# Optimization experiments

Hardware: AMD Instinct MI355X
Metric: run time of the kernel (lower is better)

The kernel has to match this reference:

```python
import jax, jax.numpy as jnp
import numpy as np

# Architecture constants (match init_kwargs)
NUM_INPUTS = 3      # 2 spatial + 1 time
NUM_SPATIAL = NUM_INPUTS - 1
NUM_LAYERS = 4      # hidden Linear(H,H) blocks
HIDDEN = 256
N_POINTS = 131072
M_DIFF = 1.0        # scalar conductivity M


def setup_inputs() -> dict:
    key = jax.random.key(0)
    ks = jax.random.split(key, 5)
    X = jax.random.uniform(ks[0], (N_POINTS, NUM_INPUTS), dtype=jnp.float32)
    # Xavier-normal weights, zero biases (matches init_method='xavier')
    W_in = jax.random.normal(ks[1], (NUM_INPUTS, HIDDEN), dtype=jnp.float32) * np.sqrt(2.0 / (NUM_INPUTS + HIDDEN))
    b_in = jnp.zeros((HIDDEN,), dtype=jnp.float32)
    W_h = jax.random.normal(ks[2], (NUM_LAYERS, HIDDEN, HIDDEN), dtype=jnp.float32) * np.sqrt(2.0 / (2 * HIDDEN))
    b_h = jnp.zeros((NUM_LAYERS, HIDDEN), dtype=jnp.float32)
    W_out = jax.random.normal(ks[3], (HIDDEN, 1), dtype=jnp.float32) * np.sqrt(2.0 / (HIDDEN + 1))
    b_out = jnp.zeros((1,), dtype=jnp.float32)
    return {"X_collocation": X, "W_in": W_in, "b_in": b_in,
            "W_h": W_h, "b_h": b_h, "W_out": W_out, "b_out": b_out}


def reference(X_collocation, W_in, b_in, W_h, b_h, W_out, b_out):
    """Faithful translation of MonodomainSolverPINNs.pde with use_ode=False,
    scalar M, no source term: residual = dv/dt - M * Laplacian_spatial(v).
    Returns (pde_loss, ode_loss)."""

    def mlp_scalar(x):  # x: [NUM_INPUTS] -> scalar v
        h = jnp.tanh(x @ W_in + b_in)
        for i in range(NUM_LAYERS):  # static small loop over layers
            h = jnp.tanh(h @ W_h[i] + b_h[i])
        return (h @ W_out + b_out)[0]

    grad_fn = jax.grad(mlp_scalar)

    def derivs(x):
        # forward-over-reverse: one reverse pass for grad, one JVP per spatial dim
        g = grad_fn(x)                       # [NUM_INPUTS]
        diag = []
        for i in range(NUM_SPATIAL):
            e = jnp.zeros((NUM_INPUTS,), dtype=x.dtype).at[i].set(1.0)
            _, hv = jax.jvp(grad_fn, (x,), (e,))
            diag.append(hv[i])               # d^2v/dx_i^2
        return g[-1], jnp.stack(diag).sum()  # dv/dt, spatial laplacian

    dv_dt, laplacian = jax.vmap(derivs)(X_collocation)  # each [N]
    diffusion = M_DIFF * laplacian
    residual = dv_dt - diffusion                        # reaction term = 0
    pde_loss = jnp.mean(residual ** 2)
    ode_loss = jnp.float32(0.0)
    return (pde_loss, ode_loss)
```

## Files before the change

kernel.cpp:

```cpp
#include <hip/hip_runtime.h>
#include <hip/hip_bf16.h>

typedef __attribute__((ext_vector_type(8))) short  short8;
typedef __attribute__((ext_vector_type(4))) float  f32x4;

#define HIDDEN   256
#define NLAYERS  4
#define NPTS     131072
#define PPW      16
#define NWG      (NPTS / PPW)
#define NSTATE   5
#define PLANE    40960

#define WS_PARTIALS   0
#define WS_WHI        65536

__device__ __forceinline__ unsigned short f2bf(float f) {
    return __builtin_bit_cast(unsigned short, __float2bfloat16(f));
}
__device__ __forceinline__ float bf2f(unsigned short h) {
    return __uint_as_float(((unsigned)h) << 16);
}
__device__ __forceinline__ unsigned pack2(float a, float b) {
    __hip_bfloat162 h2 = __float22bfloat162_rn(make_float2(a, b));
    unsigned u;
    __builtin_memcpy(&u, &h2, sizeof(u));
    return u;
}
__device__ __forceinline__ float fast_tanh(float z) {
    float e = __expf(2.f * z);
    return 1.f - __fdividef(2.f, e + 1.f);
}

__global__ void prep_w(const float* __restrict__ Wh, unsigned short* __restrict__ whi)
{
    int b    = blockIdx.x;
    int lay  = b >> 7;
    int jt   = (b >> 3) & 15;
    int kt   = b & 7;
    int lane = threadIdx.x;
    int j    = jt * 16 + (lane & 15);
    int k0   = kt * 32 + (lane >> 4) * 8;
    const float* W = Wh + lay * 65536;
    int base = ((lay * 16 + jt) * 8 + kt) * 512 + lane * 8;
#pragma unroll
    for (int e = 0; e < 8; ++e)
        whi[base + e] = f2bf(W[(k0 + e) * HIDDEN + j]);
}

__global__ __launch_bounds__(512, 4)
void pinn_mfma(const float* __restrict__ X,
               const float* __restrict__ W_in, const float* __restrict__ b_in,
               const float* __restrict__ b_h,  const float* __restrict__ W_out,
               const unsigned short* __restrict__ whi,
               double* __restrict__ partials)
{
    extern __shared__ char lds[];
    char*   P0  = lds;
    char*   P1  = lds + PLANE;
    float*  red = (float*)P1;
    double* sq  = (double*)(P1 + 2048);

    const int tid  = threadIdx.x;
    const int lane = tid & 63;
    const int swid = __builtin_amdgcn_readfirstlane(tid >> 6);
    const int q    = lane >> 4;
    const int p_   = lane & 15;
    const int wg   = blockIdx.x;
    const int pt0  = wg * PPW;

    {
        const int p   = tid & 15;
        const int jq0 = tid >> 4;
        const float* xp = X + (pt0 + p) * 3;
        const float x0 = xp[0], x1 = xp[1], x2 = xp[2];
#pragma unroll
        for (int i = 0; i < 2; ++i) {
            const int jq = jq0 + 32 * i;
            const int j0 = jq * 4;
            const f32x4 w0 = *(const f32x4*)(W_in + j0);
            const f32x4 w1 = *(const f32x4*)(W_in + HIDDEN + j0);
            const f32x4 w2 = *(const f32x4*)(W_in + 2 * HIDDEN + j0);
            const f32x4 bq = *(const f32x4*)(b_in + j0);
            float o[NSTATE][4];
#pragma unroll
            for (int r = 0; r < 4; ++r) {
                float z  = fmaf(x0, w0[r], fmaf(x1, w1[r], fmaf(x2, w2[r], bq[r])));
                float a  = fast_tanh(z);
                float td = 1.f - a * a;
                float m2 = -2.f * a * td;
                o[0][r] = a; o[1][r] = td * w0[r]; o[2][r] = td * w1[r]; o[3][r] = td * w2[r];
                o[4][r] = m2 * fmaf(w0[r], w0[r], w1[r] * w1[r]);
            }
            const int kt = j0 >> 5, kg = (j0 >> 3) & 3, e0 = j0 & 7;
            const int sub = (kg * 16 + p) * 16 + e0 * 2;
#pragma unroll
            for (int s = 0; s < NSTATE; ++s) {
                uint2 w2v = { pack2(o[s][0], o[s][1]), pack2(o[s][2], o[s][3]) };
                *(uint2*)(P0 + (s * 8 + kt) * 1024 + sub) = w2v;
            }
        }
    }
    __syncthreads();

#pragma unroll 1
    for (int l = 0; l < NLAYERS; ++l) {
        char* SP  = (l & 1) ? P1 : P0;
        char* SPn = (l & 1) ? P0 : P1;
        const char* sbase = SP + lane * 16;
        const unsigned short* wbh = whi + (l * 16 + swid * 2) * 4096 + lane * 8;

        f32x4 bias[2];
#pragma unroll
        for (int jj = 0; jj < 2; ++jj)
            bias[jj] = *(const f32x4*)(b_h + l * HIDDEN + (swid * 2 + jj) * 16 + q * 4);

        f32x4 acc[2][NSTATE];
#pragma unroll
        for (int jj = 0; jj < 2; ++jj)
#pragma unroll
            for (int mt = 0; mt < NSTATE; ++mt)
                acc[jj][mt] = (f32x4){0.f, 0.f, 0.f, 0.f};

#pragma unroll 2
        for (int kt = 0; kt < 8; ++kt) {
            short8 wh[2];
#pragma unroll
            for (int jj = 0; jj < 2; ++jj)
                wh[jj] = *(const short8*)(wbh + jj * 4096 + kt * 512);
            short8 sh_[NSTATE];
#pragma unroll
            for (int mt = 0; mt < NSTATE; ++mt)
                sh_[mt] = *(const short8*)(sbase + (mt * 8 + kt) * 1024);

            __builtin_amdgcn_s_setprio(1);
#pragma unroll
            for (int jj = 0; jj < 2; ++jj)
#pragma unroll
                for (int mt = 0; mt < NSTATE; ++mt)
                    acc[jj][mt] = __builtin_amdgcn_mfma_f32_16x16x32_bf16(wh[jj], sh_[mt], acc[jj][mt], 0, 0, 0);
            __builtin_amdgcn_s_setprio(0);
        }


#pragma unroll
        for (int jj = 0; jj < 2; ++jj) {
            const int j0 = (swid * 2 + jj) * 16 + q * 4;
            const int kt = j0 >> 5, kg = (j0 >> 3) & 3, e0 = j0 & 7;
            const int sub = (kg * 16 + p_) * 16 + e0 * 2;
            float o[NSTATE][4];
#pragma unroll
            for (int r = 0; r < 4; ++r) {
                float z0 = acc[jj][0][r] + bias[jj][r];
                float z1 = acc[jj][1][r], z2 = acc[jj][2][r];
                float z3 = acc[jj][3][r], zS = acc[jj][4][r];
                float a  = fast_tanh(z0);
                float td = 1.f - a * a;
                float m2 = -2.f * a * td;
                o[0][r] = a; o[1][r] = td * z1; o[2][r] = td * z2; o[3][r] = td * z3;
                o[4][r] = fmaf(td, zS, m2 * fmaf(z1, z1, z2 * z2));
            }
            const int sLo = (l < NLAYERS - 1) ? 0 : 3;
#pragma unroll
            for (int s = 0; s < NSTATE; ++s) {
                if (s < sLo) continue;
                uint2 w2v = { pack2(o[s][0], o[s][1]), pack2(o[s][2], o[s][3]) };
                *(uint2*)(SPn + (s * 8 + kt) * 1024 + sub) = w2v;
            }
        }
        __syncthreads();
    }

    {
        const int p   = tid & 15;
        const int jq0 = tid >> 4;
        float sum = 0.f;
#pragma unroll
        for (int i = 0; i < 2; ++i) {
            const int jq = jq0 + 32 * i, j0 = jq * 4;
            const int kt = j0 >> 5, kg = (j0 >> 3) & 3, e0 = j0 & 7;
            const int sub = (kg * 16 + p) * 16 + e0 * 2;
            uint2 gv = *(uint2*)(P0 + (3 * 8 + kt) * 1024 + sub);
            uint2 Sv = *(uint2*)(P0 + (4 * 8 + kt) * 1024 + sub);
            f32x4 wo = *(const f32x4*)(W_out + j0);
            sum = fmaf(wo[0], bf2f((unsigned short)(gv.x & 0xFFFF)) - bf2f((unsigned short)(Sv.x & 0xFFFF)), sum);
            sum = fmaf(wo[1], bf2f((unsigned short)(gv.x >> 16))    - bf2f((unsigned short)(Sv.x >> 16)),    sum);
            sum = fmaf(wo[2], bf2f((unsigned short)(gv.y & 0xFFFF)) - bf2f((unsigned short)(Sv.y & 0xFFFF)), sum);
            sum = fmaf(wo[3], bf2f((unsigned short)(gv.y >> 16))    - bf2f((unsigned short)(Sv.y >> 16)),    sum);
        }
        red[jq0 * 16 + p] = sum;
    }
    __syncthreads();
    if (tid < PPW) {
        float s = 0.f;
        for (int g = 0; g < 32; ++g) s += red[g * 16 + tid];
        double d = (double)s;
        sq[tid] = d * d;
    }
    __syncthreads();
    if (tid == 0) {
        double tot = 0.0;
        for (int p = 0; p < PPW; ++p) tot += sq[p];
        partials[wg] = tot;
    }
}

__global__ void pinn_reduce_kernel(const double* __restrict__ partials, float* __restrict__ out)
{
    __shared__ double sh[256];
    double t = 0.0;
    for (int i = 0; i < NWG / 256; ++i) t += partials[threadIdx.x * (NWG / 256) + i];
    sh[threadIdx.x] = t;
    __syncthreads();
    for (int ofs = 128; ofs > 0; ofs >>= 1) {
        if ((int)threadIdx.x < ofs) sh[threadIdx.x] += sh[threadIdx.x + ofs];
        __syncthreads();
    }
    if (threadIdx.x == 0) {
        out[0] = (float)(sh[0] / (double)NPTS);
        out[1] = 0.f;
    }
}

extern "C" void kernel_launch(void* const* d_in, const int* in_sizes, int n_in,
                              void* d_out, int out_size, void* d_ws, size_t ws_size,
                              hipStream_t stream)
{
    const float* X     = (const float*)d_in[0];
    const float* W_in  = (const float*)d_in[1];
    const float* b_in  = (const float*)d_in[2];
    const float* W_h   = (const float*)d_in[3];
    const float* b_h   = (const float*)d_in[4];
    const float* W_out = (const float*)d_in[5];

    double*         partials = (double*)((char*)d_ws + WS_PARTIALS);
    unsigned short* whi      = (unsigned short*)((char*)d_ws + WS_WHI);
    float*          out      = (float*)d_out;

    const size_t lds_bytes = 2 * PLANE;
    (void)hipFuncSetAttribute((const void*)pinn_mfma,
                              hipFuncAttributeMaxDynamicSharedMemorySize, (int)lds_bytes);

    hipLaunchKernelGGL(prep_w, dim3(512), dim3(64), 0, stream, W_h, whi);
    hipLaunchKernelGGL(pinn_mfma, dim3(NWG), dim3(512), lds_bytes, stream,
                       X, W_in, b_in, b_h, W_out, whi, partials);
    hipLaunchKernelGGL(pinn_reduce_kernel, dim3(1), dim3(256), 0, stream,
                       partials, out);
}
```

Baseline: 368.9 us.

## Fold time-derivative and Laplacian into one tangent state, single-buffer LDS

```diff
diff --git a/kernel.cpp b/kernel.cpp
--- a/kernel.cpp
+++ b/kernel.cpp
@@ -9,8 +9,8 @@
 #define NPTS     131072
 #define PPW      16
 #define NWG      (NPTS / PPW)
-#define NSTATE   5
-#define PLANE    40960
+#define NSTATE   4
+#define PLANE    32768
 
 #define WS_PARTIALS   0
 #define WS_WHI        65536
@@ -48,7 +48,7 @@
         whi[base + e] = f2bf(W[(k0 + e) * HIDDEN + j]);
 }
 
-__global__ __launch_bounds__(512, 4)
+__global__ __launch_bounds__(512, 6)
 void pinn_mfma(const float* __restrict__ X,
                const float* __restrict__ W_in, const float* __restrict__ b_in,
                const float* __restrict__ b_h,  const float* __restrict__ W_out,
@@ -56,10 +56,8 @@
                double* __restrict__ partials)
 {
     extern __shared__ char lds[];
-    char*   P0  = lds;
-    char*   P1  = lds + PLANE;
-    float*  red = (float*)P1;
-    double* sq  = (double*)(P1 + 2048);
+    float*  red = (float*)lds;
+    double* sq  = (double*)(lds + 2048);
 
     const int tid  = threadIdx.x;
     const int lane = tid & 63;
@@ -88,16 +86,19 @@
                 float z  = fmaf(x0, w0[r], fmaf(x1, w1[r], fmaf(x2, w2[r], bq[r])));
                 float a  = fast_tanh(z);
                 float td = 1.f - a * a;
-                float m2 = -2.f * a * td;
-                o[0][r] = a; o[1][r] = td * w0[r]; o[2][r] = td * w1[r]; o[3][r] = td * w2[r];
-                o[4][r] = m2 * fmaf(w0[r], w0[r], w1[r] * w1[r]);
+                float t2 = 2.f * a * td;
+                float sw = fmaf(w0[r], w0[r], w1[r] * w1[r]);
+                o[0][r] = a;
+                o[1][r] = td * w0[r];
+                o[2][r] = td * w1[r];
+                o[3][r] = fmaf(td, w2[r], t2 * sw);
             }
             const int kt = j0 >> 5, kg = (j0 >> 3) & 3, e0 = j0 & 7;
             const int sub = (kg * 16 + p) * 16 + e0 * 2;
 #pragma unroll
             for (int s = 0; s < NSTATE; ++s) {
-                uint2 w2v = { pack2(o[s][0], o[s][1]), pack2(o[s][2], o[s][3]) };
-                *(uint2*)(P0 + (s * 8 + kt) * 1024 + sub) = w2v;
+                uint2 wv = { pack2(o[s][0], o[s][1]), pack2(o[s][2], o[s][3]) };
+                *(uint2*)(lds + (s * 8 + kt) * 1024 + sub) = wv;
             }
         }
     }
@@ -105,9 +106,7 @@
 
 #pragma unroll 1
     for (int l = 0; l < NLAYERS; ++l) {
-        char* SP  = (l & 1) ? P1 : P0;
-        char* SPn = (l & 1) ? P0 : P1;
-        const char* sbase = SP + lane * 16;
+        const char* sbase = lds + lane * 16;
         const unsigned short* wbh = whi + (l * 16 + swid * 2) * 4096 + lane * 8;
 
         f32x4 bias[2];
@@ -142,6 +141,7 @@
             __builtin_amdgcn_s_setprio(0);
         }
 
+        __syncthreads();
 
 #pragma unroll
         for (int jj = 0; jj < 2; ++jj) {
@@ -152,20 +152,21 @@
 #pragma unroll
             for (int r = 0; r < 4; ++r) {
                 float z0 = acc[jj][0][r] + bias[jj][r];
-                float z1 = acc[jj][1][r], z2 = acc[jj][2][r];
-                float z3 = acc[jj][3][r], zS = acc[jj][4][r];
+                float z1 = acc[jj][1][r], z2 = acc[jj][2][r], zc = acc[jj][3][r];
                 float a  = fast_tanh(z0);
                 float td = 1.f - a * a;
-                float m2 = -2.f * a * td;
-                o[0][r] = a; o[1][r] = td * z1; o[2][r] = td * z2; o[3][r] = td * z3;
-                o[4][r] = fmaf(td, zS, m2 * fmaf(z1, z1, z2 * z2));
+                float t2 = 2.f * a * td;
+                o[0][r] = a;
+                o[1][r] = td * z1;
+                o[2][r] = td * z2;
+                o[3][r] = fmaf(td, zc, t2 * fmaf(z1, z1, z2 * z2));
             }
             const int sLo = (l < NLAYERS - 1) ? 0 : 3;
 #pragma unroll
             for (int s = 0; s < NSTATE; ++s) {
                 if (s < sLo) continue;
-                uint2 w2v = { pack2(o[s][0], o[s][1]), pack2(o[s][2], o[s][3]) };
-                *(uint2*)(SPn + (s * 8 + kt) * 1024 + sub) = w2v;
+                uint2 wv = { pack2(o[s][0], o[s][1]), pack2(o[s][2], o[s][3]) };
+                *(uint2*)(lds + (s * 8 + kt) * 1024 + sub) = wv;
             }
         }
         __syncthreads();
@@ -180,13 +181,12 @@
             const int jq = jq0 + 32 * i, j0 = jq * 4;
             const int kt = j0 >> 5, kg = (j0 >> 3) & 3, e0 = j0 & 7;
             const int sub = (kg * 16 + p) * 16 + e0 * 2;
-            uint2 gv = *(uint2*)(P0 + (3 * 8 + kt) * 1024 + sub);
-            uint2 Sv = *(uint2*)(P0 + (4 * 8 + kt) * 1024 + sub);
+            uint2 cv = *(uint2*)(lds + (3 * 8 + kt) * 1024 + sub);
             f32x4 wo = *(const f32x4*)(W_out + j0);
-            sum = fmaf(wo[0], bf2f((unsigned short)(gv.x & 0xFFFF)) - bf2f((unsigned short)(Sv.x & 0xFFFF)), sum);
-            sum = fmaf(wo[1], bf2f((unsigned short)(gv.x >> 16))    - bf2f((unsigned short)(Sv.x >> 16)),    sum);
-            sum = fmaf(wo[2], bf2f((unsigned short)(gv.y & 0xFFFF)) - bf2f((unsigned short)(Sv.y & 0xFFFF)), sum);
-            sum = fmaf(wo[3], bf2f((unsigned short)(gv.y >> 16))    - bf2f((unsigned short)(Sv.y >> 16)),    sum);
+            sum = fmaf(wo[0], bf2f((unsigned short)(cv.x & 0xFFFF)), sum);
+            sum = fmaf(wo[1], bf2f((unsigned short)(cv.x >> 16)),    sum);
+            sum = fmaf(wo[2], bf2f((unsigned short)(cv.y & 0xFFFF)), sum);
+            sum = fmaf(wo[3], bf2f((unsigned short)(cv.y >> 16)),    sum);
         }
         red[jq0 * 16 + p] = sum;
     }
@@ -237,7 +237,7 @@
     unsigned short* whi      = (unsigned short*)((char*)d_ws + WS_WHI);
     float*          out      = (float*)d_out;
 
-    const size_t lds_bytes = 2 * PLANE;
+    const size_t lds_bytes = PLANE;
     (void)hipFuncSetAttribute((const void*)pinn_mfma,
                               hipFuncAttributeMaxDynamicSharedMemorySize, (int)lds_bytes);
 
```

New measurement: 321.1 us. 13.0% less time.
